# Kernel tuning notes

Hardware: AMD Instinct MI355X
Metric: run time of the kernel (lower is better)

## Reference

```python
import jax, jax.numpy as jnp
import numpy as np

NU0 = 1.0  # nu0 temperature floor


def setup_inputs() -> dict:
    key = jax.random.key(0)
    ks = jax.random.split(key, 12)
    N, E, P, L, IN, H = 20000, 320000, 50000, 20, 128, 64
    xavier = lambda k, s: jax.random.normal(k, s, jnp.float32) * np.sqrt(2.0 / (s[0] + s[1]))
    return {
        "x": jax.random.normal(ks[0], (N, IN), jnp.float32),
        "edge_index": jax.random.randint(ks[1], (2, E), 0, N),
        "pairs": jax.random.randint(ks[2], (P, 2), 0, N),
        "gumbel": jax.random.gumbel(ks[3], (L, P, 2), jnp.float32),
        "W_enc": xavier(ks[4], (IN, H)),
        "Omega": xavier(ks[5], (H, H)),
        "Ws_raw": xavier(ks[6], (H, H)),
        "W_fc1": xavier(ks[7], (2 * H, 2 * H)),
        "W_fc2": xavier(ks[8], (2 * H, 2)),
        "W_fv": xavier(ks[9], (2 * H, 1)),
        "W_p1": xavier(ks[10], (2 * H, H)),
        "W_p2": xavier(ks[11], (H, 1)),
    }


def reference(x, edge_index, pairs, gumbel, W_enc, Omega, Ws_raw, W_fc1, W_fc2, W_fv, W_p1, W_p2):
    N = x.shape[0]
    src, dst = pairs[:, 0], pairs[:, 1]
    # add self loops
    loops = jnp.arange(N)
    row = jnp.concatenate([edge_index[0], loops])
    col = jnp.concatenate([edge_index[1], loops])
    deg = jax.ops.segment_sum(jnp.ones(col.shape, x.dtype), col, num_segments=N)
    dinv = jnp.where(deg > 0, deg, 1.0) ** -0.5 * (deg > 0)
    norm = dinv[row] * dinv[col]  # [E+N]
    Omega_as = Omega - Omega.T            # antisymmetric part
    W_s = (Ws_raw + Ws_raw.T) * 0.5       # symmetric part

    H = jax.nn.relu(x @ W_enc)                         # [N, h]
    r = jnp.concatenate([H[src], H[dst]], axis=-1)     # [P, 2h]
    ts0 = jnp.zeros(pairs.shape[0], x.dtype)

    def step(carry, g):
        H, r, ts = carry
        anti = -jax.nn.relu(H @ Omega_as)
        msg = (H @ W_s)[row] * norm[:, None]           # gather + weight
        sym = jax.ops.segment_sum(msg, col, num_segments=N)  # scatter-add
        dH = jax.nn.relu(jnp.tanh(anti + sym))
        huv = jnp.concatenate([H[src], H[dst]], axis=-1)     # [P, 2h]
        logits = jax.nn.relu(huv @ W_fc1) @ W_fc2            # [P, 2]
        nu = jax.nn.softplus(huv @ W_fv) + NU0               # [P, 1]
        c = jax.nn.softmax((logits + g) / nu, axis=-1)       # soft gumbel-softmax
        tau = c[:, :1]
        dr = jnp.concatenate([dH[src], dH[dst]], axis=-1)
        r = r + tau * dr
        H = H + dH
        ts = ts + jax.lax.stop_gradient(tau[:, 0])
        return (H, r, ts), None

    (H, r, ts), _ = jax.lax.scan(step, (H, r, ts0), gumbel)
    scores = (jax.nn.relu(r @ W_p1) @ W_p2)[:, 0]
    return scores, ts
```

## Files before the change

### kernel.cpp

```cpp
#include <hip/hip_runtime.h>
#include <math.h>


typedef short bf16x8 __attribute__((ext_vector_type(8)));
typedef float f32x4 __attribute__((ext_vector_type(4)));
typedef unsigned short u16x8 __attribute__((ext_vector_type(8)));

__device__ __forceinline__ float bf2f(unsigned short u) {
  return __uint_as_float(((unsigned)u) << 16);
}
__device__ __forceinline__ unsigned short f2bf(float f) {
  unsigned u = __float_as_uint(f);
  unsigned r = (u + 0x7FFFu + ((u >> 16) & 1u)) >> 16;
  return (unsigned short)r;
}
__device__ __forceinline__ float softplusf(float x) {
  return x > 20.f ? x : log1pf(expf(x));
}


__global__ void count_kernel(const int* __restrict__ col, int E, int* __restrict__ cnt) {
  int e = blockIdx.x * blockDim.x + threadIdx.x;
  if (e < E) atomicAdd(&cnt[col[e]], 1);
}

__global__ __launch_bounds__(1024) void scan1_kernel(int* __restrict__ cnt,
                                                     int* __restrict__ colptr,
                                                     float* __restrict__ dinv,
                                                     int* __restrict__ bsum, int N) {
  __shared__ int sh[1024];
  int t = threadIdx.x, b = blockIdx.x;
  int i = b * 1024 + t;
  int v = (i < N) ? cnt[i] : 0;
  sh[t] = v;
  __syncthreads();
  for (int off = 1; off < 1024; off <<= 1) {
    int o = (t >= off) ? sh[t - off] : 0;
    __syncthreads();
    sh[t] += o;
    __syncthreads();
  }
  if (i < N) {
    colptr[i] = sh[t] - v;
    dinv[i] = rsqrtf((float)(v + 1));
    cnt[i] = 0;
  }
  if (t == 1023) bsum[b] = sh[1023];
}

__global__ void scan2_kernel(int* __restrict__ bsum, int B) {
  if (threadIdx.x == 0 && blockIdx.x == 0) {
    int run = 0;
    for (int b = 0; b < B; b++) {
      int x = bsum[b];
      bsum[b] = run;
      run += x;
    }
    bsum[B] = run;
  }
}

__global__ void scan3_kernel(int* __restrict__ colptr, const int* __restrict__ bsum, int N) {
  int i = blockIdx.x * blockDim.x + threadIdx.x;
  if (i < N) colptr[i] += bsum[i >> 10];
  if (i == N) colptr[N] = bsum[(N + 1023) >> 10];
}

__global__ void fill_kernel(const int* __restrict__ row, const int* __restrict__ col, int E,
                            const int* __restrict__ colptr, int* __restrict__ cur,
                            int* __restrict__ csr) {
  int e = blockIdx.x * blockDim.x + threadIdx.x;
  if (e < E) {
    int c = col[e];
    int pos = colptr[c] + atomicAdd(&cur[c], 1);
    csr[pos] = row[e];
  }
}


__global__ void prep_weights(const float* __restrict__ Om, const float* __restrict__ Wsr,
                             const float* __restrict__ Wfc1, const float* __restrict__ Wenc,
                             const float* __restrict__ Wp1, unsigned short* __restrict__ Wn2T,
                             unsigned short* __restrict__ Wn2Tlo,
                             unsigned short* __restrict__ Wfc1T,
                             unsigned short* __restrict__ WencT,
                             unsigned short* __restrict__ Wp1T) {
  int idx = blockIdx.x * blockDim.x + threadIdx.x;
  if (idx < 128 * 64) {
    int j = idx / 64, k = idx % 64;
    float v;
    if (j < 64) {
      v = Om[k * 64 + j] - Om[j * 64 + k];
    } else {
      int jj = j - 64;
      v = 0.5f * (Wsr[k * 64 + jj] + Wsr[jj * 64 + k]);
    }
    unsigned short hi = f2bf(v);
    Wn2T[idx] = hi;
    Wn2Tlo[idx] = f2bf(v - bf2f(hi));
  } else if (idx < 128 * 64 + 128 * 128) {
    int t = idx - 128 * 64;
    int j = t / 128, k = t % 128;
    Wfc1T[t] = f2bf(Wfc1[k * 128 + j]);
  } else if (idx < 128 * 64 + 128 * 128 + 64 * 128) {
    int t = idx - 128 * 64 - 128 * 128;
    int j = t / 128, k = t % 128;
    WencT[t] = f2bf(Wenc[k * 64 + j]);
  } else if (idx < 128 * 64 + 128 * 128 + 2 * 64 * 128) {
    int t = idx - 128 * 64 - 128 * 128 - 64 * 128;
    int j = t / 128, k = t % 128;
    Wp1T[t] = f2bf(Wp1[k * 64 + j]);
  }
}


__global__ __launch_bounds__(256) void enc_gemm(const float* __restrict__ X,
                                                const unsigned short* __restrict__ WT,
                                                float* __restrict__ H, float* __restrict__ H0,
                                                unsigned short* __restrict__ Hb_hi,
                                                unsigned short* __restrict__ Hb_lo, int N) {
  int gw = blockIdx.x * 4 + (threadIdx.x >> 6);
  int l = threadIdx.x & 63;
  int r0 = gw * 16;
  if (r0 >= N) return;
  int arow = min(r0 + (l & 15), N - 1);
  int ak = (l >> 4) * 8;
  bf16x8 a[4];
#pragma unroll
  for (int kk = 0; kk < 4; kk++) {
    const float* xp = X + (size_t)arow * 128 + kk * 32 + ak;
    float4 u = *(const float4*)xp;
    float4 v = *(const float4*)(xp + 4);
    bf16x8 t;
    t[0] = (short)f2bf(u.x); t[1] = (short)f2bf(u.y);
    t[2] = (short)f2bf(u.z); t[3] = (short)f2bf(u.w);
    t[4] = (short)f2bf(v.x); t[5] = (short)f2bf(v.y);
    t[6] = (short)f2bf(v.z); t[7] = (short)f2bf(v.w);
    a[kk] = t;
  }
  int rbase = r0 + (l >> 4) * 4;
#pragma unroll
  for (int c = 0; c < 4; c++) {
    const unsigned short* wp = WT + (size_t)(c * 16 + (l & 15)) * 128 + ak;
    f32x4 acc = {0.f, 0.f, 0.f, 0.f};
#pragma unroll
    for (int kk = 0; kk < 4; kk++)
      acc = __builtin_amdgcn_mfma_f32_16x16x32_bf16(a[kk], *(const bf16x8*)(wp + kk * 32), acc,
                                                    0, 0, 0);
    int gcol = c * 16 + (l & 15);
#pragma unroll
    for (int b = 0; b < 4; b++) {
      int gr = rbase + b;
      if (gr < N) {
        float v = fmaxf(acc[b], 0.f);
        H[(size_t)gr * 64 + gcol] = v;
        H0[(size_t)gr * 64 + gcol] = v;
        unsigned short hi = f2bf(v);
        Hb_hi[(size_t)gr * 64 + gcol] = hi;
        Hb_lo[(size_t)gr * 64 + gcol] = f2bf(v - bf2f(hi));
      }
    }
  }
}


__global__ __launch_bounds__(256) void node_gemm(const unsigned short* __restrict__ Hb_hi,
                                                 const unsigned short* __restrict__ Hb_lo,
                                                 const unsigned short* __restrict__ Wn2T,
                                                 const unsigned short* __restrict__ Wn2Tlo,
                                                 const float* __restrict__ H,
                                                 const float* __restrict__ Wfv,
                                                 const float* __restrict__ dinv,
                                                 float* __restrict__ Abuf,
                                                 float* __restrict__ Bsbuf,
                                                 float* __restrict__ ftfb, int N) {
  int gw = blockIdx.x * 4 + (threadIdx.x >> 6);
  int l = threadIdx.x & 63;
  int r0 = gw * 16;
  if (r0 >= N) return;
  int arow = min(r0 + (l & 15), N - 1);
  int ak = (l >> 4) * 8;
  bf16x8 a0h = *(const bf16x8*)(Hb_hi + (size_t)arow * 64 + ak);
  bf16x8 a1h = *(const bf16x8*)(Hb_hi + (size_t)arow * 64 + 32 + ak);
  bf16x8 a0l = *(const bf16x8*)(Hb_lo + (size_t)arow * 64 + ak);
  bf16x8 a1l = *(const bf16x8*)(Hb_lo + (size_t)arow * 64 + 32 + ak);
  int rbase = r0 + (l >> 4) * 4;
  float dv[4];
#pragma unroll
  for (int b = 0; b < 4; b++) dv[b] = dinv[min(rbase + b, N - 1)];
#pragma unroll
  for (int c = 0; c < 8; c++) {
    size_t woff = (size_t)(c * 16 + (l & 15)) * 64 + ak;
    bf16x8 b0h = *(const bf16x8*)(Wn2T + woff);
    bf16x8 b1h = *(const bf16x8*)(Wn2T + woff + 32);
    bf16x8 b0l = *(const bf16x8*)(Wn2Tlo + woff);
    bf16x8 b1l = *(const bf16x8*)(Wn2Tlo + woff + 32);
    f32x4 acc = {0.f, 0.f, 0.f, 0.f};
    acc = __builtin_amdgcn_mfma_f32_16x16x32_bf16(a0h, b0h, acc, 0, 0, 0);
    acc = __builtin_amdgcn_mfma_f32_16x16x32_bf16(a1h, b1h, acc, 0, 0, 0);
    acc = __builtin_amdgcn_mfma_f32_16x16x32_bf16(a0l, b0h, acc, 0, 0, 0);
    acc = __builtin_amdgcn_mfma_f32_16x16x32_bf16(a1l, b1h, acc, 0, 0, 0);
    acc = __builtin_amdgcn_mfma_f32_16x16x32_bf16(a0h, b0l, acc, 0, 0, 0);
    acc = __builtin_amdgcn_mfma_f32_16x16x32_bf16(a1h, b1l, acc, 0, 0, 0);
    int gcol = c * 16 + (l & 15);
#pragma unroll
    for (int b = 0; b < 4; b++) {
      int gr = rbase + b;
      if (gr < N) {
        float v = acc[b];
        if (c >= 4) Bsbuf[(size_t)gr * 64 + (gcol - 64)] = v * dv[b];
        else Abuf[(size_t)gr * 64 + gcol] = v;
      }
    }
  }
  int d0 = (l >> 4) * 16;
  const float* hp = H + (size_t)arow * 64 + d0;
  float p0 = 0.f, p1 = 0.f;
#pragma unroll
  for (int i = 0; i < 16; i += 4) {
    float4 h = *(const float4*)(hp + i);
    p0 += h.x * Wfv[d0 + i] + h.y * Wfv[d0 + i + 1] + h.z * Wfv[d0 + i + 2] +
          h.w * Wfv[d0 + i + 3];
    p1 += h.x * Wfv[64 + d0 + i] + h.y * Wfv[64 + d0 + i + 1] + h.z * Wfv[64 + d0 + i + 2] +
          h.w * Wfv[64 + d0 + i + 3];
  }
  p0 += __shfl_xor(p0, 16, 64);
  p0 += __shfl_xor(p0, 32, 64);
  p1 += __shfl_xor(p1, 16, 64);
  p1 += __shfl_xor(p1, 32, 64);
  if (l < 16 && r0 + l < N) {
    ftfb[2 * (r0 + l)] = p0;
    ftfb[2 * (r0 + l) + 1] = p1;
  }
}


__global__ __launch_bounds__(256) void step_fused(
    const float* __restrict__ A_cur, const float* __restrict__ Bs_cur,
    float* __restrict__ A_nxt, float* __restrict__ Bs_nxt, const int* __restrict__ colptr,
    const int* __restrict__ csr, const float* __restrict__ dinv, float* __restrict__ H,
    const unsigned short* __restrict__ Hc_hi, const unsigned short* __restrict__ Hc_lo,
    unsigned short* __restrict__ Hn_hi, unsigned short* __restrict__ Hn_lo,
    unsigned short* __restrict__ dHall, const unsigned short* __restrict__ Wn2T,
    const unsigned short* __restrict__ Wn2Tlo, const unsigned short* __restrict__ Wfc1T,
    const float* __restrict__ Wfc2, const float* __restrict__ ftfb_cur,
    float* __restrict__ ftfb_nxt, const float* __restrict__ Wfv,
    const int* __restrict__ pairs, const float* __restrict__ gum, float* __restrict__ tau,
    int t, int LT, int N, int P, int PB) {
  __shared__ unsigned short ldsHi[16 * 72];
  __shared__ unsigned short ldsLo[16 * 72];
  int l = threadIdx.x & 63;
  int w = threadIdx.x >> 6;
  if ((int)blockIdx.x < PB) {
    int p0 = ((int)blockIdx.x * 4 + w) * 16;
    if (p0 >= P) return;
    int pr = min(p0 + (l & 15), P - 1);
    int src = pairs[2 * pr], dst = pairs[2 * pr + 1];
    bf16x8 ah[4], al[4];
#pragma unroll
    for (int kk = 0; kk < 4; kk++) {
      int k0 = kk * 32 + (l >> 4) * 8;
      size_t base = (k0 < 64) ? ((size_t)src * 64 + k0) : ((size_t)dst * 64 + (k0 - 64));
      ah[kk] = *(const bf16x8*)(Hc_hi + base);
      al[kk] = *(const bf16x8*)(Hc_lo + base);
    }
    float l0[4] = {0.f, 0.f, 0.f, 0.f};
    float l1[4] = {0.f, 0.f, 0.f, 0.f};
#pragma unroll
    for (int c = 0; c < 8; c++) {
      const unsigned short* wp = Wfc1T + (size_t)(c * 16 + (l & 15)) * 128 + (l >> 4) * 8;
      f32x4 acc = {0.f, 0.f, 0.f, 0.f};
#pragma unroll
      for (int kk = 0; kk < 4; kk++) {
        bf16x8 wv = *(const bf16x8*)(wp + kk * 32);
        acc = __builtin_amdgcn_mfma_f32_16x16x32_bf16(ah[kk], wv, acc, 0, 0, 0);
        acc = __builtin_amdgcn_mfma_f32_16x16x32_bf16(al[kk], wv, acc, 0, 0, 0);
      }
      int m = c * 16 + (l & 15);
      float w0 = Wfc2[2 * m], w1 = Wfc2[2 * m + 1];
#pragma unroll
      for (int b = 0; b < 4; b++) {
        float zz = fmaxf(acc[b], 0.f);
        l0[b] = fmaf(zz, w0, l0[b]);
        l1[b] = fmaf(zz, w1, l1[b]);
      }
    }
#pragma unroll
    for (int off = 1; off < 16; off <<= 1) {
#pragma unroll
      for (int b = 0; b < 4; b++) {
        l0[b] += __shfl_xor(l0[b], off, 64);
        l1[b] += __shfl_xor(l1[b], off, 64);
      }
    }
    int li = l & 15;
    if (li < 4) {
      int pg = p0 + (l >> 4) * 4 + li;
      if (pg < P) {
        int s2 = pairs[2 * pg], d2 = pairs[2 * pg + 1];
        float nu = softplusf(ftfb_cur[2 * s2] + ftfb_cur[2 * d2 + 1]) + 1.0f;
        float g0 = gum[2 * (size_t)pg], g1 = gum[2 * (size_t)pg + 1];
        float dlt = ((l1[li] + g1) - (l0[li] + g0)) / nu;
        tau[(size_t)pg * LT + t] = 1.0f / (1.0f + expf(dlt));
      }
    }
  } else {
    int nb0 = ((int)blockIdx.x - PB) * 16;
    int g = l >> 4;
    int node = nb0 + w * 4 + g;
    int q = (l & 15) * 4;
    bool valid = node < N;
    float4 hn = make_float4(0.f, 0.f, 0.f, 0.f);
    if (valid) {
      size_t base = (size_t)node * 64 + q;
      float4 v = *(const float4*)(Bs_cur + base);
      float aa0 = v.x, aa1 = v.y, aa2 = v.z, aa3 = v.w;
      int beg = colptr[node], end = colptr[node + 1];
      int i = beg;
      for (; i + 3 < end; i += 4) {
        int n0 = csr[i], n1 = csr[i + 1], n2 = csr[i + 2], n3 = csr[i + 3];
        float4 u0 = *(const float4*)(Bs_cur + (size_t)n0 * 64 + q);
        float4 u1 = *(const float4*)(Bs_cur + (size_t)n1 * 64 + q);
        float4 u2 = *(const float4*)(Bs_cur + (size_t)n2 * 64 + q);
        float4 u3 = *(const float4*)(Bs_cur + (size_t)n3 * 64 + q);
        aa0 += (u0.x + u1.x) + (u2.x + u3.x);
        aa1 += (u0.y + u1.y) + (u2.y + u3.y);
        aa2 += (u0.z + u1.z) + (u2.z + u3.z);
        aa3 += (u0.w + u1.w) + (u2.w + u3.w);
      }
      for (; i < end; i++) {
        int n0 = csr[i];
        float4 u0 = *(const float4*)(Bs_cur + (size_t)n0 * 64 + q);
        aa0 += u0.x; aa1 += u0.y; aa2 += u0.z; aa3 += u0.w;
      }
      float dval = dinv[node];
      float4 av = *(const float4*)(A_cur + base);
      float dh0 = fmaxf(tanhf(dval * aa0 - fmaxf(av.x, 0.f)), 0.f);
      float dh1 = fmaxf(tanhf(dval * aa1 - fmaxf(av.y, 0.f)), 0.f);
      float dh2 = fmaxf(tanhf(dval * aa2 - fmaxf(av.z, 0.f)), 0.f);
      float dh3 = fmaxf(tanhf(dval * aa3 - fmaxf(av.w, 0.f)), 0.f);
      ushort4 od;
      od.x = f2bf(dh0); od.y = f2bf(dh1); od.z = f2bf(dh2); od.w = f2bf(dh3);
      *(ushort4*)(dHall + (size_t)node * (LT * 64) + t * 64 + q) = od;
      float* hp = H + base;
      float4 h = *(const float4*)hp;
      hn.x = h.x + dh0; hn.y = h.y + dh1; hn.z = h.z + dh2; hn.w = h.w + dh3;
      *(float4*)hp = hn;
    }
    ushort4 whi, wlo;
    whi.x = f2bf(hn.x); wlo.x = f2bf(hn.x - bf2f(whi.x));
    whi.y = f2bf(hn.y); wlo.y = f2bf(hn.y - bf2f(whi.y));
    whi.z = f2bf(hn.z); wlo.z = f2bf(hn.z - bf2f(whi.z));
    whi.w = f2bf(hn.w); wlo.w = f2bf(hn.w - bf2f(whi.w));
    int r = w * 4 + g;
    *(ushort4*)(ldsHi + r * 72 + q) = whi;
    *(ushort4*)(ldsLo + r * 72 + q) = wlo;
    if (valid) {
      *(ushort4*)(Hn_hi + (size_t)node * 64 + q) = whi;
      *(ushort4*)(Hn_lo + (size_t)node * 64 + q) = wlo;
    }
    float p0 = hn.x * Wfv[q] + hn.y * Wfv[q + 1] + hn.z * Wfv[q + 2] + hn.w * Wfv[q + 3];
    float p1 = hn.x * Wfv[64 + q] + hn.y * Wfv[64 + q + 1] + hn.z * Wfv[64 + q + 2] +
               hn.w * Wfv[64 + q + 3];
#pragma unroll
    for (int off = 1; off < 16; off <<= 1) {
      p0 += __shfl_xor(p0, off, 64);
      p1 += __shfl_xor(p1, off, 64);
    }
    if ((l & 15) == 0 && valid) {
      ftfb_nxt[2 * node] = p0;
      ftfb_nxt[2 * node + 1] = p1;
    }
    __syncthreads();
    int rowA = l & 15;
    int ak = g * 8;
    bf16x8 a0h = *(const bf16x8*)(ldsHi + rowA * 72 + ak);
    bf16x8 a1h = *(const bf16x8*)(ldsHi + rowA * 72 + 32 + ak);
    bf16x8 a0l = *(const bf16x8*)(ldsLo + rowA * 72 + ak);
    bf16x8 a1l = *(const bf16x8*)(ldsLo + rowA * 72 + 32 + ak);
    float dv[4];
#pragma unroll
    for (int b = 0; b < 4; b++) dv[b] = dinv[min(nb0 + g * 4 + b, N - 1)];
#pragma unroll
    for (int cc = 0; cc < 2; cc++) {
      int c = w * 2 + cc;
      size_t woff = (size_t)(c * 16 + rowA) * 64 + ak;
      bf16x8 b0h = *(const bf16x8*)(Wn2T + woff);
      bf16x8 b1h = *(const bf16x8*)(Wn2T + woff + 32);
      bf16x8 b0l = *(const bf16x8*)(Wn2Tlo + woff);
      bf16x8 b1l = *(const bf16x8*)(Wn2Tlo + woff + 32);
      f32x4 acc = {0.f, 0.f, 0.f, 0.f};
      acc = __builtin_amdgcn_mfma_f32_16x16x32_bf16(a0h, b0h, acc, 0, 0, 0);
      acc = __builtin_amdgcn_mfma_f32_16x16x32_bf16(a1h, b1h, acc, 0, 0, 0);
      acc = __builtin_amdgcn_mfma_f32_16x16x32_bf16(a0l, b0h, acc, 0, 0, 0);
      acc = __builtin_amdgcn_mfma_f32_16x16x32_bf16(a1l, b1h, acc, 0, 0, 0);
      acc = __builtin_amdgcn_mfma_f32_16x16x32_bf16(a0h, b0l, acc, 0, 0, 0);
      acc = __builtin_amdgcn_mfma_f32_16x16x32_bf16(a1h, b1l, acc, 0, 0, 0);
      int gcol = c * 16 + rowA;
#pragma unroll
      for (int b = 0; b < 4; b++) {
        int gr = nb0 + g * 4 + b;
        if (gr < N) {
          float v = acc[b];
          if (c >= 4) Bs_nxt[(size_t)gr * 64 + (gcol - 64)] = v * dv[b];
          else A_nxt[(size_t)gr * 64 + gcol] = v;
        }
      }
    }
  }
}


__global__ __launch_bounds__(256) void rbuild_kernel(
    const float* __restrict__ H0, const unsigned short* __restrict__ dHall,
    const float* __restrict__ tau, const int* __restrict__ pairs,
    unsigned short* __restrict__ rb_hi, unsigned short* __restrict__ rb_lo,
    float* __restrict__ ts, int P, int N, int Lsteps) {
  int p = blockIdx.x * 16 + (threadIdx.x >> 4);
  int l = threadIdx.x & 15;
  if (p >= P) return;
  int node = (l < 8) ? pairs[2 * p] : pairs[2 * p + 1];
  int d0 = (l & 7) * 8;
  const float* hp = H0 + (size_t)node * 64 + d0;
  float4 h0 = *(const float4*)hp;
  float4 h1 = *(const float4*)(hp + 4);
  float acc[8] = {h0.x, h0.y, h0.z, h0.w, h1.x, h1.y, h1.z, h1.w};
  float tsum = 0.f;
  const unsigned short* dbase = dHall + (size_t)node * (Lsteps * 64) + d0;
  const float* taup = tau + (size_t)p * Lsteps;
#pragma unroll 4
  for (int t = 0; t < Lsteps; t++) {
    float tt = taup[t];
    tsum += tt;
    u16x8 v = *(const u16x8*)(dbase + t * 64);
#pragma unroll
    for (int i = 0; i < 8; i++) acc[i] = fmaf(tt, bf2f(v[i]), acc[i]);
  }
  u16x8 ohi, olo;
#pragma unroll
  for (int i = 0; i < 8; i++) {
    unsigned short hi = f2bf(acc[i]);
    ohi[i] = hi;
    olo[i] = f2bf(acc[i] - bf2f(hi));
  }
  *(u16x8*)(rb_hi + (size_t)p * 128 + l * 8) = ohi;
  *(u16x8*)(rb_lo + (size_t)p * 128 + l * 8) = olo;
  if (l == 0) ts[p] = tsum;
}


__global__ __launch_bounds__(256) void final_gemm(const unsigned short* __restrict__ rb_hi,
                                                  const unsigned short* __restrict__ rb_lo,
                                                  const unsigned short* __restrict__ WT,
                                                  const float* __restrict__ Wp2,
                                                  float* __restrict__ out, int P) {
  int gw = blockIdx.x * 4 + (threadIdx.x >> 6);
  int l = threadIdx.x & 63;
  int r0 = gw * 16;
  if (r0 >= P) return;
  int arow = min(r0 + (l & 15), P - 1);
  int ak = (l >> 4) * 8;
  bf16x8 ah[4], al[4];
#pragma unroll
  for (int kk = 0; kk < 4; kk++) {
    ah[kk] = *(const bf16x8*)(rb_hi + (size_t)arow * 128 + kk * 32 + ak);
    al[kk] = *(const bf16x8*)(rb_lo + (size_t)arow * 128 + kk * 32 + ak);
  }
  float s[4] = {0.f, 0.f, 0.f, 0.f};
#pragma unroll
  for (int c = 0; c < 4; c++) {
    const unsigned short* wp = WT + (size_t)(c * 16 + (l & 15)) * 128 + ak;
    f32x4 acc = {0.f, 0.f, 0.f, 0.f};
#pragma unroll
    for (int kk = 0; kk < 4; kk++) {
      bf16x8 wv = *(const bf16x8*)(wp + kk * 32);
      acc = __builtin_amdgcn_mfma_f32_16x16x32_bf16(ah[kk], wv, acc, 0, 0, 0);
      acc = __builtin_amdgcn_mfma_f32_16x16x32_bf16(al[kk], wv, acc, 0, 0, 0);
    }
    float w = Wp2[c * 16 + (l & 15)];
#pragma unroll
    for (int b = 0; b < 4; b++) s[b] = fmaf(fmaxf(acc[b], 0.f), w, s[b]);
  }
#pragma unroll
  for (int off = 1; off < 16; off <<= 1) {
#pragma unroll
    for (int b = 0; b < 4; b++) s[b] += __shfl_xor(s[b], off, 64);
  }
  if ((l & 15) == 0) {
    int rbase = r0 + (l >> 4) * 4;
#pragma unroll
    for (int b = 0; b < 4; b++) {
      int gr = rbase + b;
      if (gr < P) out[gr] = s[b];
    }
  }
}


extern "C" void kernel_launch(void* const* d_in, const int* in_sizes, int n_in, void* d_out,
                              int out_size, void* d_ws, size_t ws_size, hipStream_t stream) {
  const float* x = (const float*)d_in[0];
  const int* edge = (const int*)d_in[1];
  const int* pairs = (const int*)d_in[2];
  const float* gumbel = (const float*)d_in[3];
  const float* Wenc = (const float*)d_in[4];
  const float* Om = (const float*)d_in[5];
  const float* Wsr = (const float*)d_in[6];
  const float* Wfc1 = (const float*)d_in[7];
  const float* Wfc2 = (const float*)d_in[8];
  const float* Wfv = (const float*)d_in[9];
  const float* Wp1 = (const float*)d_in[10];
  const float* Wp2 = (const float*)d_in[11];
  const int IN = 128;
  const int N = in_sizes[0] / IN;
  const int E = in_sizes[1] / 2;
  const int P = in_sizes[2] / 2;
  const int L = in_sizes[3] / (2 * P);
  float* out = (float*)d_out;

  char* wsb = (char*)d_ws;
  size_t off = 0;
  auto alloc = [&](size_t bytes) -> char* {
    char* p = wsb + off;
    off = (off + bytes + 255) & ~(size_t)255;
    return p;
  };
  const int NB = (N + 1023) >> 10;
  float* dinv = (float*)alloc((size_t)N * 4);
  int* cnt = (int*)alloc((size_t)N * 4);
  int* colptr = (int*)alloc((size_t)(N + 1) * 4);
  int* bsum = (int*)alloc((size_t)(NB + 1) * 4);
  int* csr = (int*)alloc((size_t)E * 4);
  unsigned short* Wn2T = (unsigned short*)alloc((size_t)128 * 64 * 2);
  unsigned short* Wn2Tlo = (unsigned short*)alloc((size_t)128 * 64 * 2);
  unsigned short* Wfc1T = (unsigned short*)alloc((size_t)128 * 128 * 2);
  unsigned short* WencT = (unsigned short*)alloc((size_t)64 * 128 * 2);
  unsigned short* Wp1T = (unsigned short*)alloc((size_t)64 * 128 * 2);
  float* H = (float*)alloc((size_t)N * 64 * 4);
  float* H0 = (float*)alloc((size_t)N * 64 * 4);
  unsigned short* HbA_hi = (unsigned short*)alloc((size_t)N * 64 * 2);
  unsigned short* HbA_lo = (unsigned short*)alloc((size_t)N * 64 * 2);
  unsigned short* HbB_hi = (unsigned short*)alloc((size_t)N * 64 * 2);
  unsigned short* HbB_lo = (unsigned short*)alloc((size_t)N * 64 * 2);
  float* A_a = (float*)alloc((size_t)N * 64 * 4);
  float* A_b = (float*)alloc((size_t)N * 64 * 4);
  float* Bs_a = (float*)alloc((size_t)N * 64 * 4);
  float* Bs_b = (float*)alloc((size_t)N * 64 * 4);
  float* ftfbA = (float*)alloc((size_t)N * 2 * 4);
  float* ftfbB = (float*)alloc((size_t)N * 2 * 4);
  unsigned short* dHall = (unsigned short*)alloc((size_t)N * L * 64 * 2);
  float* tau = (float*)alloc((size_t)P * L * 4);
  unsigned short* rb_hi = (unsigned short*)alloc((size_t)P * 128 * 2);
  unsigned short* rb_lo = (unsigned short*)alloc((size_t)P * 128 * 2);
  (void)ws_size;
  (void)n_in;
  (void)out_size;

  const int* erow = edge;
  const int* ecol = edge + E;

  hipMemsetAsync(cnt, 0, (size_t)N * 4, stream);
  count_kernel<<<(E + 255) / 256, 256, 0, stream>>>(ecol, E, cnt);
  scan1_kernel<<<NB, 1024, 0, stream>>>(cnt, colptr, dinv, bsum, N);
  scan2_kernel<<<1, 64, 0, stream>>>(bsum, NB);
  scan3_kernel<<<(N + 256) / 256, 256, 0, stream>>>(colptr, bsum, N);
  fill_kernel<<<(E + 255) / 256, 256, 0, stream>>>(erow, ecol, E, colptr, cnt, csr);
  prep_weights<<<(128 * 64 + 128 * 128 + 2 * 64 * 128 + 255) / 256, 256, 0, stream>>>(
      Om, Wsr, Wfc1, Wenc, Wp1, Wn2T, Wn2Tlo, Wfc1T, WencT, Wp1T);

  int nwaves = (N + 15) / 16;
  enc_gemm<<<(nwaves + 3) / 4, 256, 0, stream>>>(x, WencT, H, H0, HbA_hi, HbA_lo, N);
  node_gemm<<<(nwaves + 3) / 4, 256, 0, stream>>>(HbA_hi, HbA_lo, Wn2T, Wn2Tlo, H, Wfv, dinv,
                                                  A_a, Bs_a, ftfbA, N);

  unsigned short* cur_hi = HbA_hi;
  unsigned short* cur_lo = HbA_lo;
  unsigned short* nxt_hi = HbB_hi;
  unsigned short* nxt_lo = HbB_lo;
  float* A_cur = A_a;
  float* A_nxt = A_b;
  float* Bs_cur = Bs_a;
  float* Bs_nxt = Bs_b;
  float* ff_cur = ftfbA;
  float* ff_nxt = ftfbB;
  const int PB = (P + 63) / 64;
  const int AGB = (N + 15) / 16;
  for (int t = 0; t < L; t++) {
    step_fused<<<PB + AGB, 256, 0, stream>>>(
        A_cur, Bs_cur, A_nxt, Bs_nxt, colptr, csr, dinv, H, cur_hi, cur_lo, nxt_hi, nxt_lo,
        dHall, Wn2T, Wn2Tlo, Wfc1T, Wfc2, ff_cur, ff_nxt, Wfv, pairs,
        gumbel + (size_t)t * P * 2, tau, t, L, N, P, PB);
    { unsigned short* tmp = cur_hi; cur_hi = nxt_hi; nxt_hi = tmp; }
    { unsigned short* tmp = cur_lo; cur_lo = nxt_lo; nxt_lo = tmp; }
    { float* tmp = A_cur; A_cur = A_nxt; A_nxt = tmp; }
    { float* tmp = Bs_cur; Bs_cur = Bs_nxt; Bs_nxt = tmp; }
    { float* tmp = ff_cur; ff_cur = ff_nxt; ff_nxt = tmp; }
  }
  rbuild_kernel<<<(P + 15) / 16, 256, 0, stream>>>(H0, dHall, tau, pairs, rb_hi, rb_lo,
                                                   out + P, P, N, L);
  int pwaves = (P + 15) / 16;
  final_gemm<<<(pwaves + 3) / 4, 256, 0, stream>>>(rb_hi, rb_lo, Wp1T, Wp2, out, P);
}
```

Baseline: 936.4 us.

## Precompute per-node fc1 projections instead of per-pair fc1 GEMM

Splits huv@W_fc1 into H[src]@W_top + H[dst]@W_bot, computing per-node T and D projections (N x 128 each) inside the node-update GEMM. The pair branch then only gathers two 128-float rows, adds them, applies relu and dots with W_fc2, so the per-pair MFMA work (P > N) goes away. This adds 2x N x 128 fp32 writes and reads per step and removes the bf16 H copy buffers. The fc1 product now uses the hi/lo split on H but not on the weights, which may slightly change numerics.

```diff
diff --git a/kernel.cpp b/kernel.cpp
--- a/kernel.cpp
+++ b/kernel.cpp
@@ -164,16 +164,13 @@
 }
 
 
-__global__ __launch_bounds__(256) void node_gemm(const unsigned short* __restrict__ Hb_hi,
-                                                 const unsigned short* __restrict__ Hb_lo,
-                                                 const unsigned short* __restrict__ Wn2T,
-                                                 const unsigned short* __restrict__ Wn2Tlo,
-                                                 const float* __restrict__ H,
-                                                 const float* __restrict__ Wfv,
-                                                 const float* __restrict__ dinv,
-                                                 float* __restrict__ Abuf,
-                                                 float* __restrict__ Bsbuf,
-                                                 float* __restrict__ ftfb, int N) {
+__global__ __launch_bounds__(256) void node_gemm(
+    const unsigned short* __restrict__ Hb_hi, const unsigned short* __restrict__ Hb_lo,
+    const unsigned short* __restrict__ Wn2T, const unsigned short* __restrict__ Wn2Tlo,
+    const unsigned short* __restrict__ Wfc1T, const float* __restrict__ H,
+    const float* __restrict__ Wfv, const float* __restrict__ dinv, float* __restrict__ Abuf,
+    float* __restrict__ Bsbuf, float* __restrict__ Tbuf, float* __restrict__ Dbuf,
+    float* __restrict__ ftfb, int N) {
   int gw = blockIdx.x * 4 + (threadIdx.x >> 6);
   int l = threadIdx.x & 63;
   int r0 = gw * 16;
@@ -213,6 +210,25 @@
       }
     }
   }
+#pragma unroll
+  for (int c = 0; c < 16; c++) {
+    int j = ((c & 7) * 16 + (l & 15));
+    int koff = (c < 8) ? 0 : 64;
+    const unsigned short* wp = Wfc1T + (size_t)j * 128 + koff + ak;
+    bf16x8 b0 = *(const bf16x8*)(wp);
+    bf16x8 b1 = *(const bf16x8*)(wp + 32);
+    f32x4 acc = {0.f, 0.f, 0.f, 0.f};
+    acc = __builtin_amdgcn_mfma_f32_16x16x32_bf16(a0h, b0, acc, 0, 0, 0);
+    acc = __builtin_amdgcn_mfma_f32_16x16x32_bf16(a1h, b1, acc, 0, 0, 0);
+    acc = __builtin_amdgcn_mfma_f32_16x16x32_bf16(a0l, b0, acc, 0, 0, 0);
+    acc = __builtin_amdgcn_mfma_f32_16x16x32_bf16(a1l, b1, acc, 0, 0, 0);
+    float* dstb = (c < 8) ? Tbuf : Dbuf;
+#pragma unroll
+    for (int b = 0; b < 4; b++) {
+      int gr = rbase + b;
+      if (gr < N) dstb[(size_t)gr * 128 + j] = acc[b];
+    }
+  }
   int d0 = (l >> 4) * 16;
   const float* hp = H + (size_t)arow * 64 + d0;
   float p0 = 0.f, p1 = 0.f;
@@ -237,72 +253,57 @@
 
 __global__ __launch_bounds__(256) void step_fused(
     const float* __restrict__ A_cur, const float* __restrict__ Bs_cur,
-    float* __restrict__ A_nxt, float* __restrict__ Bs_nxt, const int* __restrict__ colptr,
-    const int* __restrict__ csr, const float* __restrict__ dinv, float* __restrict__ H,
-    const unsigned short* __restrict__ Hc_hi, const unsigned short* __restrict__ Hc_lo,
-    unsigned short* __restrict__ Hn_hi, unsigned short* __restrict__ Hn_lo,
-    unsigned short* __restrict__ dHall, const unsigned short* __restrict__ Wn2T,
-    const unsigned short* __restrict__ Wn2Tlo, const unsigned short* __restrict__ Wfc1T,
-    const float* __restrict__ Wfc2, const float* __restrict__ ftfb_cur,
-    float* __restrict__ ftfb_nxt, const float* __restrict__ Wfv,
-    const int* __restrict__ pairs, const float* __restrict__ gum, float* __restrict__ tau,
-    int t, int LT, int N, int P, int PB) {
+    const float* __restrict__ T_cur, const float* __restrict__ D_cur,
+    float* __restrict__ A_nxt, float* __restrict__ Bs_nxt, float* __restrict__ T_nxt,
+    float* __restrict__ D_nxt, const int* __restrict__ colptr, const int* __restrict__ csr,
+    const float* __restrict__ dinv, float* __restrict__ H, unsigned short* __restrict__ dHall,
+    const unsigned short* __restrict__ Wn2T, const unsigned short* __restrict__ Wn2Tlo,
+    const unsigned short* __restrict__ Wfc1T, const float* __restrict__ Wfc2,
+    const float* __restrict__ ftfb_cur, float* __restrict__ ftfb_nxt,
+    const float* __restrict__ Wfv, const int* __restrict__ pairs,
+    const float* __restrict__ gum, float* __restrict__ tau, int t, int LT, int N, int P,
+    int PB) {
   __shared__ unsigned short ldsHi[16 * 72];
   __shared__ unsigned short ldsLo[16 * 72];
   int l = threadIdx.x & 63;
   int w = threadIdx.x >> 6;
   if ((int)blockIdx.x < PB) {
-    int p0 = ((int)blockIdx.x * 4 + w) * 16;
-    if (p0 >= P) return;
-    int pr = min(p0 + (l & 15), P - 1);
-    int src = pairs[2 * pr], dst = pairs[2 * pr + 1];
-    bf16x8 ah[4], al[4];
-#pragma unroll
-    for (int kk = 0; kk < 4; kk++) {
-      int k0 = kk * 32 + (l >> 4) * 8;
-      size_t base = (k0 < 64) ? ((size_t)src * 64 + k0) : ((size_t)dst * 64 + (k0 - 64));
-      ah[kk] = *(const bf16x8*)(Hc_hi + base);
-      al[kk] = *(const bf16x8*)(Hc_lo + base);
-    }
-    float l0[4] = {0.f, 0.f, 0.f, 0.f};
-    float l1[4] = {0.f, 0.f, 0.f, 0.f};
-#pragma unroll
-    for (int c = 0; c < 8; c++) {
-      const unsigned short* wp = Wfc1T + (size_t)(c * 16 + (l & 15)) * 128 + (l >> 4) * 8;
-      f32x4 acc = {0.f, 0.f, 0.f, 0.f};
-#pragma unroll
-      for (int kk = 0; kk < 4; kk++) {
-        bf16x8 wv = *(const bf16x8*)(wp + kk * 32);
-        acc = __builtin_amdgcn_mfma_f32_16x16x32_bf16(ah[kk], wv, acc, 0, 0, 0);
-        acc = __builtin_amdgcn_mfma_f32_16x16x32_bf16(al[kk], wv, acc, 0, 0, 0);
-      }
-      int m = c * 16 + (l & 15);
-      float w0 = Wfc2[2 * m], w1 = Wfc2[2 * m + 1];
-#pragma unroll
-      for (int b = 0; b < 4; b++) {
-        float zz = fmaxf(acc[b], 0.f);
-        l0[b] = fmaf(zz, w0, l0[b]);
-        l1[b] = fmaf(zz, w1, l1[b]);
-      }
-    }
-#pragma unroll
-    for (int off = 1; off < 16; off <<= 1) {
-#pragma unroll
-      for (int b = 0; b < 4; b++) {
-        l0[b] += __shfl_xor(l0[b], off, 64);
-        l1[b] += __shfl_xor(l1[b], off, 64);
-      }
-    }
-    int li = l & 15;
-    if (li < 4) {
-      int pg = p0 + (l >> 4) * 4 + li;
-      if (pg < P) {
-        int s2 = pairs[2 * pg], d2 = pairs[2 * pg + 1];
-        float nu = softplusf(ftfb_cur[2 * s2] + ftfb_cur[2 * d2 + 1]) + 1.0f;
-        float g0 = gum[2 * (size_t)pg], g1 = gum[2 * (size_t)pg + 1];
-        float dlt = ((l1[li] + g1) - (l0[li] + g0)) / nu;
-        tau[(size_t)pg * LT + t] = 1.0f / (1.0f + expf(dlt));
-      }
+    int p = (int)blockIdx.x * 32 + w * 8 + (l >> 3);
+    bool act = p < P;
+    int pc = act ? p : P - 1;
+    int src = pairs[2 * pc], dst = pairs[2 * pc + 1];
+    int d0 = (l & 7) * 16;
+    const float* Tp = T_cur + (size_t)src * 128 + d0;
+    const float* Dp = D_cur + (size_t)dst * 128 + d0;
+    float l0 = 0.f, l1 = 0.f;
+#pragma unroll
+    for (int i = 0; i < 16; i += 4) {
+      float4 tv = *(const float4*)(Tp + i);
+      float4 dv4 = *(const float4*)(Dp + i);
+      float z0 = fmaxf(tv.x + dv4.x, 0.f);
+      float z1 = fmaxf(tv.y + dv4.y, 0.f);
+      float z2 = fmaxf(tv.z + dv4.z, 0.f);
+      float z3 = fmaxf(tv.w + dv4.w, 0.f);
+      int m = d0 + i;
+      l0 = fmaf(z0, Wfc2[2 * m], l0);
+      l1 = fmaf(z0, Wfc2[2 * m + 1], l1);
+      l0 = fmaf(z1, Wfc2[2 * m + 2], l0);
+      l1 = fmaf(z1, Wfc2[2 * m + 3], l1);
+      l0 = fmaf(z2, Wfc2[2 * m + 4], l0);
+      l1 = fmaf(z2, Wfc2[2 * m + 5], l1);
+      l0 = fmaf(z3, Wfc2[2 * m + 6], l0);
+      l1 = fmaf(z3, Wfc2[2 * m + 7], l1);
+    }
+#pragma unroll
+    for (int off = 1; off < 8; off <<= 1) {
+      l0 += __shfl_xor(l0, off, 64);
+      l1 += __shfl_xor(l1, off, 64);
+    }
+    if ((l & 7) == 0 && act) {
+      float nu = softplusf(ftfb_cur[2 * src] + ftfb_cur[2 * dst + 1]) + 1.0f;
+      float g0 = gum[2 * (size_t)p], g1 = gum[2 * (size_t)p + 1];
+      float dlt = ((l1 + g1) - (l0 + g0)) / nu;
+      tau[(size_t)p * LT + t] = 1.0f / (1.0f + expf(dlt));
     }
   } else {
     int nb0 = ((int)blockIdx.x - PB) * 16;
@@ -355,10 +356,6 @@
     int r = w * 4 + g;
     *(ushort4*)(ldsHi + r * 72 + q) = whi;
     *(ushort4*)(ldsLo + r * 72 + q) = wlo;
-    if (valid) {
-      *(ushort4*)(Hn_hi + (size_t)node * 64 + q) = whi;
-      *(ushort4*)(Hn_lo + (size_t)node * 64 + q) = wlo;
-    }
     float p0 = hn.x * Wfv[q] + hn.y * Wfv[q + 1] + hn.z * Wfv[q + 2] + hn.w * Wfv[q + 3];
     float p1 = hn.x * Wfv[64 + q] + hn.y * Wfv[64 + q + 1] + hn.z * Wfv[64 + q + 2] +
                hn.w * Wfv[64 + q + 3];
@@ -383,7 +380,7 @@
     for (int b = 0; b < 4; b++) dv[b] = dinv[min(nb0 + g * 4 + b, N - 1)];
 #pragma unroll
     for (int cc = 0; cc < 2; cc++) {
-      int c = w * 2 + cc;
+      int c = cc * 4 + w;
       size_t woff = (size_t)(c * 16 + rowA) * 64 + ak;
       bf16x8 b0h = *(const bf16x8*)(Wn2T + woff);
       bf16x8 b1h = *(const bf16x8*)(Wn2T + woff + 32);
@@ -402,9 +399,29 @@
         int gr = nb0 + g * 4 + b;
         if (gr < N) {
           float v = acc[b];
-          if (c >= 4) Bs_nxt[(size_t)gr * 64 + (gcol - 64)] = v * dv[b];
+          if (cc == 1) Bs_nxt[(size_t)gr * 64 + (gcol - 64)] = v * dv[b];
           else A_nxt[(size_t)gr * 64 + gcol] = v;
         }
+      }
+    }
+#pragma unroll
+    for (int cc = 0; cc < 4; cc++) {
+      int jb = (cc & 1) + 2 * w;
+      int koff = (cc < 2) ? 0 : 64;
+      int j = jb * 16 + rowA;
+      const unsigned short* wp = Wfc1T + (size_t)j * 128 + koff + ak;
+      bf16x8 b0 = *(const bf16x8*)(wp);
+      bf16x8 b1 = *(const bf16x8*)(wp + 32);
+      f32x4 acc = {0.f, 0.f, 0.f, 0.f};
+      acc = __builtin_amdgcn_mfma_f32_16x16x32_bf16(a0h, b0, acc, 0, 0, 0);
+      acc = __builtin_amdgcn_mfma_f32_16x16x32_bf16(a1h, b1, acc, 0, 0, 0);
+      acc = __builtin_amdgcn_mfma_f32_16x16x32_bf16(a0l, b0, acc, 0, 0, 0);
+      acc = __builtin_amdgcn_mfma_f32_16x16x32_bf16(a1l, b1, acc, 0, 0, 0);
+      float* dstb = (cc < 2) ? T_nxt : D_nxt;
+#pragma unroll
+      for (int b = 0; b < 4; b++) {
+        int gr = nb0 + g * 4 + b;
+        if (gr < N) dstb[(size_t)gr * 128 + j] = acc[b];
       }
     }
   }
@@ -538,14 +555,16 @@
   unsigned short* Wp1T = (unsigned short*)alloc((size_t)64 * 128 * 2);
   float* H = (float*)alloc((size_t)N * 64 * 4);
   float* H0 = (float*)alloc((size_t)N * 64 * 4);
-  unsigned short* HbA_hi = (unsigned short*)alloc((size_t)N * 64 * 2);
-  unsigned short* HbA_lo = (unsigned short*)alloc((size_t)N * 64 * 2);
-  unsigned short* HbB_hi = (unsigned short*)alloc((size_t)N * 64 * 2);
-  unsigned short* HbB_lo = (unsigned short*)alloc((size_t)N * 64 * 2);
+  unsigned short* Hb_hi = (unsigned short*)alloc((size_t)N * 64 * 2);
+  unsigned short* Hb_lo = (unsigned short*)alloc((size_t)N * 64 * 2);
   float* A_a = (float*)alloc((size_t)N * 64 * 4);
   float* A_b = (float*)alloc((size_t)N * 64 * 4);
   float* Bs_a = (float*)alloc((size_t)N * 64 * 4);
   float* Bs_b = (float*)alloc((size_t)N * 64 * 4);
+  float* T_a = (float*)alloc((size_t)N * 128 * 4);
+  float* T_b = (float*)alloc((size_t)N * 128 * 4);
+  float* D_a = (float*)alloc((size_t)N * 128 * 4);
+  float* D_b = (float*)alloc((size_t)N * 128 * 4);
   float* ftfbA = (float*)alloc((size_t)N * 2 * 4);
   float* ftfbB = (float*)alloc((size_t)N * 2 * 4);
   unsigned short* dHall = (unsigned short*)alloc((size_t)N * L * 64 * 2);
@@ -569,31 +588,27 @@
       Om, Wsr, Wfc1, Wenc, Wp1, Wn2T, Wn2Tlo, Wfc1T, WencT, Wp1T);
 
   int nwaves = (N + 15) / 16;
-  enc_gemm<<<(nwaves + 3) / 4, 256, 0, stream>>>(x, WencT, H, H0, HbA_hi, HbA_lo, N);
-  node_gemm<<<(nwaves + 3) / 4, 256, 0, stream>>>(HbA_hi, HbA_lo, Wn2T, Wn2Tlo, H, Wfv, dinv,
-                                                  A_a, Bs_a, ftfbA, N);
-
-  unsigned short* cur_hi = HbA_hi;
-  unsigned short* cur_lo = HbA_lo;
-  unsigned short* nxt_hi = HbB_hi;
-  unsigned short* nxt_lo = HbB_lo;
-  float* A_cur = A_a;
-  float* A_nxt = A_b;
-  float* Bs_cur = Bs_a;
-  float* Bs_nxt = Bs_b;
+  enc_gemm<<<(nwaves + 3) / 4, 256, 0, stream>>>(x, WencT, H, H0, Hb_hi, Hb_lo, N);
+  node_gemm<<<(nwaves + 3) / 4, 256, 0, stream>>>(Hb_hi, Hb_lo, Wn2T, Wn2Tlo, Wfc1T, H, Wfv,
+                                                  dinv, A_a, Bs_a, T_a, D_a, ftfbA, N);
+
+  float* A_cur = A_a;   float* A_nxt = A_b;
+  float* Bs_cur = Bs_a; float* Bs_nxt = Bs_b;
+  float* T_cur = T_a;   float* T_nxt = T_b;
+  float* D_cur = D_a;   float* D_nxt = D_b;
   float* ff_cur = ftfbA;
   float* ff_nxt = ftfbB;
-  const int PB = (P + 63) / 64;
+  const int PB = (P + 31) / 32;
   const int AGB = (N + 15) / 16;
   for (int t = 0; t < L; t++) {
     step_fused<<<PB + AGB, 256, 0, stream>>>(
-        A_cur, Bs_cur, A_nxt, Bs_nxt, colptr, csr, dinv, H, cur_hi, cur_lo, nxt_hi, nxt_lo,
-        dHall, Wn2T, Wn2Tlo, Wfc1T, Wfc2, ff_cur, ff_nxt, Wfv, pairs,
-        gumbel + (size_t)t * P * 2, tau, t, L, N, P, PB);
-    { unsigned short* tmp = cur_hi; cur_hi = nxt_hi; nxt_hi = tmp; }
-    { unsigned short* tmp = cur_lo; cur_lo = nxt_lo; nxt_lo = tmp; }
+        A_cur, Bs_cur, T_cur, D_cur, A_nxt, Bs_nxt, T_nxt, D_nxt, colptr, csr, dinv, H, dHall,
+        Wn2T, Wn2Tlo, Wfc1T, Wfc2, ff_cur, ff_nxt, Wfv, pairs, gumbel + (size_t)t * P * 2, tau,
+        t, L, N, P, PB);
     { float* tmp = A_cur; A_cur = A_nxt; A_nxt = tmp; }
     { float* tmp = Bs_cur; Bs_cur = Bs_nxt; Bs_nxt = tmp; }
+    { float* tmp = T_cur; T_cur = T_nxt; T_nxt = tmp; }
+    { float* tmp = D_cur; D_cur = D_nxt; D_nxt = tmp; }
     { float* tmp = ff_cur; ff_cur = ff_nxt; ff_nxt = tmp; }
   }
   rbuild_kernel<<<(P + 15) / 16, 256, 0, stream>>>(H0, dHall, tau, pairs, rb_hi, rb_lo,
```

Result: faster. 917.4 us (-2.0%).
